# Kernel optimization log

Hardware: AMD Instinct MI355X
Metric: run time of the kernel (lower is better)

The kernel has to match this reference:

```python
import jax, jax.numpy as jnp
import numpy as np

B, T, D_OBS, D_ACT, H = 1024, 1024, 32, 4, 64


def setup_inputs() -> dict:
    key = jax.random.key(0)
    ks = jax.random.split(key, 8)
    s = 0.1
    obs = jax.random.normal(ks[0], (B, T, D_OBS), dtype=jnp.float32)
    action = jax.random.normal(ks[1], (B, T, D_ACT), dtype=jnp.float32)
    # GRUCell params (torch layout): weight_ih [3H, Din], weight_hh [3H, H]
    W_ih = jax.random.normal(ks[2], (3 * H, D_OBS + D_ACT), dtype=jnp.float32) * s
    W_hh = jax.random.normal(ks[3], (3 * H, H), dtype=jnp.float32) * s
    b_ih = jax.random.normal(ks[4], (3 * H,), dtype=jnp.float32) * s
    b_hh = jax.random.normal(ks[5], (3 * H,), dtype=jnp.float32) * s
    # reward head: Linear(H, 1)
    W_r = jax.random.normal(ks[6], (1, H), dtype=jnp.float32) * s
    b_r = jax.random.normal(ks[7], (1,), dtype=jnp.float32) * s
    return {"obs": obs, "action": action, "W_ih": W_ih, "b_ih": b_ih,
            "W_hh": W_hh, "b_hh": b_hh, "W_r": W_r, "b_r": b_r}


def reference(obs, action, W_ih, b_ih, W_hh, b_hh, W_r, b_r):
    # x_t = cat(obs_t, action_t); GRUCell recurrence; reward = Linear(h_t)
    x = jnp.concatenate([obs, action], axis=-1)              # [B, T, Din]
    # Precompute input-to-hidden gates for all timesteps (batched GEMM)
    gi = jnp.einsum('btd,gd->btg', x, W_ih) + b_ih           # [B, T, 3H]
    gi_t = jnp.swapaxes(gi, 0, 1)                            # [T, B, 3H]

    def step(h, gi_step):
        gh = h @ W_hh.T + b_hh                               # [B, 3H]
        ghr, ghz, ghn = jnp.split(gh, 3, axis=-1)
        gir, giz, gin = jnp.split(gi_step, 3, axis=-1)
        r = jax.nn.sigmoid(gir + ghr)
        z = jax.nn.sigmoid(giz + ghz)
        n = jnp.tanh(gin + r * ghn)
        h_new = (1.0 - z) * n + z * h
        reward = h_new @ W_r.T + b_r                         # [B, 1]
        return h_new, reward

    h0 = jnp.zeros((obs.shape[0], H), dtype=obs.dtype)
    h_final, rewards = jax.lax.scan(step, h0, gi_t)          # rewards: [T, B, 1]
    return h_final, jnp.swapaxes(rewards, 0, 1)              # h: [B, H], reward: [B, T, 1]
```

## Files before the change

kernel.cpp:

```cpp
#include <hip/hip_runtime.h>


#define BB 1024
#define TT 1024
#define DOBS 32
#define DACT 4
#define HH 64

typedef __attribute__((ext_vector_type(8))) short short8;
typedef __attribute__((ext_vector_type(4))) float f32x4;

#define MFMA(A, B, C) __builtin_amdgcn_mfma_f32_16x16x32_bf16((A), (B), (C), 0, 0, 0)

static __device__ __forceinline__ unsigned short f2bf(float f) {
    unsigned u = __float_as_uint(f);
    u += 0x7fffu + ((u >> 16) & 1u);
    return (unsigned short)(u >> 16);
}
static __device__ __forceinline__ float frcp(float x) { return __builtin_amdgcn_rcpf(x); }
static __device__ __forceinline__ unsigned cvt_pk(float lo, float hi) {
    unsigned r;
    asm("v_cvt_pk_bf16_f32 %0, %1, %2" : "=v"(r) : "v"(lo), "v"(hi));
    return r;
}

#define L2E 1.442695040888963f

__global__ __launch_bounds__(256)
void pack_x(const float* __restrict__ obs, const float* __restrict__ act,
            unsigned short* __restrict__ xext)
{
    const size_t r = (size_t)blockIdx.x * 256 + threadIdx.x;
    const float* o = obs + r * DOBS;
    unsigned short* d = xext + r * 40;
    short8 v[5];
#pragma unroll
    for (int j = 0; j < 4; ++j) {
        float4 a = ((const float4*)o)[2 * j];
        float4 b = ((const float4*)o)[2 * j + 1];
        short8 t;
        t[0]=f2bf(a.x); t[1]=f2bf(a.y); t[2]=f2bf(a.z); t[3]=f2bf(a.w);
        t[4]=f2bf(b.x); t[5]=f2bf(b.y); t[6]=f2bf(b.z); t[7]=f2bf(b.w);
        v[j] = t;
    }
    {
        float4 a = *(const float4*)(act + r * DACT);
        short8 t;
        t[0]=f2bf(a.x); t[1]=f2bf(a.y); t[2]=f2bf(a.z); t[3]=f2bf(a.w);
        t[4]=(short)0x3f80; t[5]=0; t[6]=0; t[7]=0;
        v[4] = t;
    }
#pragma unroll
    for (int j = 0; j < 5; ++j) ((short8*)d)[j] = v[j];
}

#define LOADX(XO, XA, T)                                                       \
  {                                                                            \
    if (PACKED) {                                                              \
      XO = *(const short8*)(px + (size_t)(T) * 40 + 8 * q);                    \
      XA = (q == 0) ? *(const short8*)(px + (size_t)(T) * 40 + 32) : zero8;    \
    } else {                                                                   \
      const int tc_ = (T) < TT ? (T) : TT - 1;                                 \
      const float* op_ = po + (size_t)tc_ * DOBS + 8 * q;                      \
      float4 a_ = *(const float4*)op_, b_ = *(const float4*)(op_ + 4);         \
      short8 f_;                                                               \
      f_[0]=f2bf(a_.x); f_[1]=f2bf(a_.y); f_[2]=f2bf(a_.z); f_[3]=f2bf(a_.w);  \
      f_[4]=f2bf(b_.x); f_[5]=f2bf(b_.y); f_[6]=f2bf(b_.z); f_[7]=f2bf(b_.w);  \
      XO = f_;                                                                 \
      if (q == 0) {                                                            \
        float4 av_ = *(const float4*)(pa + (size_t)tc_ * DACT);                \
        short8 g_;                                                             \
        g_[0]=f2bf(av_.x); g_[1]=f2bf(av_.y); g_[2]=f2bf(av_.z);               \
        g_[3]=f2bf(av_.w); g_[4]=(short)0x3f80; g_[5]=0; g_[6]=0; g_[7]=0;     \
        XA = g_;                                                               \
      } else XA = zero8;                                                       \
    }                                                                          \
  }

#define STEP(XO, XA, CR_, CZ_, CN_, PH, T)                                     \
  {                                                                            \
    short8 Ah0 = *(const short8*)((const char*)hbuf[PH] + rdaddr0);            \
    short8 Ah1 = *(const short8*)((const char*)hbuf[PH] + rdaddr1);            \
    f32x4 cr_ = CR_, cz_ = CZ_, cni_ = CN_;        \
    CR_ = MFMA(AX[0][1], XA, MFMA(AX[0][0], XO, zf));    \
    CZ_ = MFMA(AX[1][1], XA, MFMA(AX[1][0], XO, zf));                          \
    CN_ = MFMA(AX[2][1], XA, MFMA(AX[2][0], XO, zf));                          \
    LOADX(XO, XA, (T) + 4)                            \
    f32x4 Cr  = MFMA(AH[0][1], Ah1, MFMA(AH[0][0], Ah0, cr_));                 \
    f32x4 Cz  = MFMA(AH[1][1], Ah1, MFMA(AH[1][0], Ah0, cz_));                 \
    f32x4 Cnh = MFMA(AH[2][1], Ah1, MFMA(AH[2][0], Ah0, bhn4));                \
    f32x4 Crw = zf;                                                            \
    if (w == 3) Crw = MFMA(AR[1], Ah1, MFMA(AR[0], Ah0, zf));                  \
    _Pragma("unroll")                                                          \
    for (int reg = 0; reg < 4; ++reg) {                                        \
      float rr   = frcp(1.0f + __builtin_amdgcn_exp2f(Cr[reg]));               \
      float zz   = frcp(1.0f + __builtin_amdgcn_exp2f(Cz[reg]));               \
      float E    = __builtin_amdgcn_exp2f(__builtin_fmaf(rr, Cnh[reg], cni_[reg])); \
      float nn   = __builtin_fmaf(-2.0f, frcp(E + 1.0f), 1.0f);                \
      hold[reg]  = __builtin_fmaf(zz, hold[reg] - nn, nn);                     \
    }                                                                          \
    unsigned pk0 = cvt_pk(hold[0], hold[1]);                                   \
    unsigned pk1 = cvt_pk(hold[2], hold[3]);                                   \
    *(uint2*)((char*)hbuf[PH ^ 1] + wraddr) = make_uint2(pk0, pk1);            \
    if (w == 3 && q == 0 && (T) > 0)                                           \
      rew[(size_t)(bid * 16 + c) * TT + (T) - 1] = Crw[0] + brr;               \
    asm volatile("s_waitcnt lgkmcnt(0)" ::: "memory");                         \
    __builtin_amdgcn_s_barrier();                                              \
    asm volatile("" ::: "memory");                                             \
  }

template<bool PACKED>
__global__ __launch_bounds__(256, 1)
void gru_fused(const unsigned short* __restrict__ xext,
               const float* __restrict__ obs, const float* __restrict__ act,
               const float* __restrict__ W_ih, const float* __restrict__ b_ih,
               const float* __restrict__ W_hh, const float* __restrict__ b_hh,
               const float* __restrict__ W_r, const float* __restrict__ b_r,
               float* __restrict__ out)
{
    const int tid = threadIdx.x;
    const int w = tid >> 6, l = tid & 63, c = l & 15, q = l >> 4;
    const int bid = blockIdx.x;
    const int u0 = 16 * w + 4 * q;

    __shared__ __align__(16) unsigned short hbuf[2][16 * 64];

    short8 AX[3][2], AH[3][2];
#pragma unroll
    for (int m = 0; m < 3; ++m) {
        const float sc = (m == 2) ? (2.0f * L2E) : (-L2E);
        const int j = w + 4 * m;
        const int g = 16 * j + c;
        {
            const float* wp = W_ih + (size_t)g * 36 + 8 * q;
            float4 a = *(const float4*)wp, b = *(const float4*)(wp + 4);
            short8 f;
            f[0]=f2bf(a.x*sc); f[1]=f2bf(a.y*sc); f[2]=f2bf(a.z*sc); f[3]=f2bf(a.w*sc);
            f[4]=f2bf(b.x*sc); f[5]=f2bf(b.y*sc); f[6]=f2bf(b.z*sc); f[7]=f2bf(b.w*sc);
            AX[m][0] = f;
        }
        {
            short8 f;
#pragma unroll
            for (int i = 0; i < 8; ++i) {
                int k = 32 + 8 * q + i;
                float v = 0.f;
                if (k < 36)       v = W_ih[(size_t)g * 36 + k];
                else if (k == 36) v = b_ih[g] + (g < 128 ? b_hh[g] : 0.f);
                f[i] = f2bf(v * sc);
            }
            AX[m][1] = f;
        }
#pragma unroll
        for (int kk = 0; kk < 2; ++kk) {
            const float* wp = W_hh + (size_t)g * HH + 32 * kk + 8 * q;
            float4 a = *(const float4*)wp, b = *(const float4*)(wp + 4);
            short8 f;
            f[0]=f2bf(a.x*sc); f[1]=f2bf(a.y*sc); f[2]=f2bf(a.z*sc); f[3]=f2bf(a.w*sc);
            f[4]=f2bf(b.x*sc); f[5]=f2bf(b.y*sc); f[6]=f2bf(b.z*sc); f[7]=f2bf(b.w*sc);
            AH[m][kk] = f;
        }
    }
    short8 AR[2];
#pragma unroll
    for (int kk = 0; kk < 2; ++kk) {
        short8 f;
#pragma unroll
        for (int i = 0; i < 8; ++i) {
            int k = 32 * kk + 8 * q + i;
            f[i] = (c == 0) ? (short)f2bf(W_r[k]) : (short)0;
        }
        AR[kk] = f;
    }

    f32x4 bhn4;
#pragma unroll
    for (int reg = 0; reg < 4; ++reg) bhn4[reg] = b_hh[128 + u0 + reg] * (2.0f * L2E);
    const float brr = b_r[0];

    const int swz = c & 7;
    const int wraddr  = c * 128 + ((((u0 >> 3)) ^ swz) << 4) + (u0 & 7) * 2;
    const int rdaddr0 = c * 128 + ((q ^ swz) << 4);
    const int rdaddr1 = c * 128 + (((4 + q) ^ swz) << 4);

    const size_t row = (size_t)(bid * 16 + c) * TT;
    const unsigned short* px = xext + row * 40;
    const float* po = obs + row * DOBS;
    const float* pa = act + row * DACT;

    const short8 zero8 = {0, 0, 0, 0, 0, 0, 0, 0};
    const f32x4 zf = {0.f, 0.f, 0.f, 0.f};

    ((uint2*)hbuf[0])[tid] = make_uint2(0u, 0u);
    short8 xoA, xaA, xoB, xaB;
    LOADX(xoA, xaA, 0)
    LOADX(xoB, xaB, 1)
    f32x4 cgrA = MFMA(AX[0][1], xaA, MFMA(AX[0][0], xoA, zf));
    f32x4 cgzA = MFMA(AX[1][1], xaA, MFMA(AX[1][0], xoA, zf));
    f32x4 cgnA = MFMA(AX[2][1], xaA, MFMA(AX[2][0], xoA, zf));
    f32x4 cgrB = MFMA(AX[0][1], xaB, MFMA(AX[0][0], xoB, zf));
    f32x4 cgzB = MFMA(AX[1][1], xaB, MFMA(AX[1][0], xoB, zf));
    f32x4 cgnB = MFMA(AX[2][1], xaB, MFMA(AX[2][0], xoB, zf));
    LOADX(xoA, xaA, 2)
    LOADX(xoB, xaB, 3)
    float hold[4] = {0.f, 0.f, 0.f, 0.f};
    asm volatile("s_waitcnt lgkmcnt(0)" ::: "memory");
    __builtin_amdgcn_s_barrier();
    asm volatile("" ::: "memory");

    float* rew = out + (size_t)BB * HH;

#pragma unroll 1
    for (int t = 0; t < TT; t += 4) {
        STEP(xoA, xaA, cgrA, cgzA, cgnA, 0, t)
        STEP(xoB, xaB, cgrB, cgzB, cgnB, 1, t + 1)
        STEP(xoA, xaA, cgrA, cgzA, cgnA, 0, t + 2)
        STEP(xoB, xaB, cgrB, cgzB, cgnB, 1, t + 3)
    }

    if (w == 3) {
        short8 Ah0 = *(const short8*)((const char*)hbuf[0] + rdaddr0);
        short8 Ah1 = *(const short8*)((const char*)hbuf[0] + rdaddr1);
        f32x4 Crw = MFMA(AR[0], Ah0, zf);
        Crw = MFMA(AR[1], Ah1, Crw);
        if (q == 0)
            rew[(size_t)(bid * 16 + c) * TT + TT - 1] = Crw[0] + brr;
    }
    *(float4*)(out + (size_t)(bid * 16 + c) * HH + u0) =
        make_float4(hold[0], hold[1], hold[2], hold[3]);
}

extern "C" void kernel_launch(void* const* d_in, const int* in_sizes, int n_in,
                              void* d_out, int out_size, void* d_ws, size_t ws_size,
                              hipStream_t stream)
{
    const float* obs    = (const float*)d_in[0];
    const float* action = (const float*)d_in[1];
    const float* W_ih   = (const float*)d_in[2];
    const float* b_ih   = (const float*)d_in[3];
    const float* W_hh   = (const float*)d_in[4];
    const float* b_hh   = (const float*)d_in[5];
    const float* W_r    = (const float*)d_in[6];
    const float* b_r    = (const float*)d_in[7];
    float* out          = (float*)d_out;

    const size_t xext_bytes = ((size_t)BB * TT + 8) * 40 * sizeof(unsigned short);
    if (ws_size >= xext_bytes) {
        unsigned short* xext = (unsigned short*)d_ws;
        pack_x<<<dim3((BB * TT) / 256), dim3(256), 0, stream>>>(obs, action, xext);
        gru_fused<true><<<dim3(BB / 16), dim3(256), 0, stream>>>(
            xext, obs, action, W_ih, b_ih, W_hh, b_hh, W_r, b_r, out);
    } else {
        gru_fused<false><<<dim3(BB / 16), dim3(256), 0, stream>>>(
            nullptr, obs, action, W_ih, b_ih, W_hh, b_hh, W_r, b_r, out);
    }
}
```

Baseline: 415.3 us.

## Split GRU block into two alternating wave sets that ping-pong timesteps

Doubles the block to 512 threads, arranged as two 256-thread sets that take turns. One set runs the recurrent MFMA and gate step for one timestep while the other computes the input projection and loads x for its next step. The hidden state now moves between the sets through an extra fp32 shared buffer, because each set only holds every other step's state in registers. The reward-head work is also rotated across waves by iteration. The aim is to take input loads and projections off the serial critical path, at the cost of more LDS traffic and two barriers per timestep pair.

```diff
diff --git a/kernel.cpp b/kernel.cpp
--- a/kernel.cpp
+++ b/kernel.cpp
@@ -77,40 +77,44 @@
     }                                                                          \
   }
 
-#define STEP(XO, XA, CR_, CZ_, CN_, PH, T)                                     \
+#define HEAVY(PH, T, IT)                                                       \
   {                                                                            \
     short8 Ah0 = *(const short8*)((const char*)hbuf[PH] + rdaddr0);            \
     short8 Ah1 = *(const short8*)((const char*)hbuf[PH] + rdaddr1);            \
-    f32x4 cr_ = CR_, cz_ = CZ_, cni_ = CN_;        \
-    CR_ = MFMA(AX[0][1], XA, MFMA(AX[0][0], XO, zf));    \
-    CZ_ = MFMA(AX[1][1], XA, MFMA(AX[1][0], XO, zf));                          \
-    CN_ = MFMA(AX[2][1], XA, MFMA(AX[2][0], XO, zf));                          \
-    LOADX(XO, XA, (T) + 4)                            \
-    f32x4 Cr  = MFMA(AH[0][1], Ah1, MFMA(AH[0][0], Ah0, cr_));                 \
-    f32x4 Cz  = MFMA(AH[1][1], Ah1, MFMA(AH[1][0], Ah0, cz_));                 \
+    f32x4 hp = *(const f32x4*)((const char*)hf32[PH] + f32addr);               \
+    f32x4 Cr  = MFMA(AH[0][1], Ah1, MFMA(AH[0][0], Ah0, cgr));                 \
+    f32x4 Cz  = MFMA(AH[1][1], Ah1, MFMA(AH[1][0], Ah0, cgz));                 \
     f32x4 Cnh = MFMA(AH[2][1], Ah1, MFMA(AH[2][0], Ah0, bhn4));                \
     f32x4 Crw = zf;                                                            \
-    if (w == 3) Crw = MFMA(AR[1], Ah1, MFMA(AR[0], Ah0, zf));                  \
+    const bool dorw_ = (w == ((IT) & 3));                                      \
+    if (dorw_) Crw = MFMA(AR[1], Ah1, MFMA(AR[0], Ah0, zf));                   \
     _Pragma("unroll")                                                          \
     for (int reg = 0; reg < 4; ++reg) {                                        \
       float rr   = frcp(1.0f + __builtin_amdgcn_exp2f(Cr[reg]));               \
       float zz   = frcp(1.0f + __builtin_amdgcn_exp2f(Cz[reg]));               \
-      float E    = __builtin_amdgcn_exp2f(__builtin_fmaf(rr, Cnh[reg], cni_[reg])); \
+      float E    = __builtin_amdgcn_exp2f(__builtin_fmaf(rr, Cnh[reg], cgn[reg])); \
       float nn   = __builtin_fmaf(-2.0f, frcp(E + 1.0f), 1.0f);                \
-      hold[reg]  = __builtin_fmaf(zz, hold[reg] - nn, nn);                     \
+      hold[reg]  = __builtin_fmaf(zz, hp[reg] - nn, nn);                       \
     }                                                                          \
     unsigned pk0 = cvt_pk(hold[0], hold[1]);                                   \
     unsigned pk1 = cvt_pk(hold[2], hold[3]);                                   \
     *(uint2*)((char*)hbuf[PH ^ 1] + wraddr) = make_uint2(pk0, pk1);            \
-    if (w == 3 && q == 0 && (T) > 0)                                           \
+    *(f32x4*)((char*)hf32[PH ^ 1] + f32addr) = hold;                           \
+    if (dorw_ && q == 0 && (T) > 0)                                            \
       rew[(size_t)(bid * 16 + c) * TT + (T) - 1] = Crw[0] + brr;               \
     asm volatile("s_waitcnt lgkmcnt(0)" ::: "memory");                         \
-    __builtin_amdgcn_s_barrier();                                              \
-    asm volatile("" ::: "memory");                                             \
   }
 
+#define LIGHT(T2)                                                              \
+  {                                                                            \
+    cgr = MFMA(AX[0][1], xa, MFMA(AX[0][0], xo, zf));                          \
+    cgz = MFMA(AX[1][1], xa, MFMA(AX[1][0], xo, zf));                          \
+    cgn = MFMA(AX[2][1], xa, MFMA(AX[2][0], xo, zf));                          \
+    LOADX(xo, xa, (T2) + 2)                                                    \
+  }
+
 template<bool PACKED>
-__global__ __launch_bounds__(256, 1)
+__global__ __launch_bounds__(512, 1)
 void gru_fused(const unsigned short* __restrict__ xext,
                const float* __restrict__ obs, const float* __restrict__ act,
                const float* __restrict__ W_ih, const float* __restrict__ b_ih,
@@ -119,11 +123,14 @@
                float* __restrict__ out)
 {
     const int tid = threadIdx.x;
-    const int w = tid >> 6, l = tid & 63, c = l & 15, q = l >> 4;
+    const int set = tid >> 8;
+    const int w = (tid >> 6) & 3;
+    const int l = tid & 63, c = l & 15, q = l >> 4;
     const int bid = blockIdx.x;
     const int u0 = 16 * w + 4 * q;
 
     __shared__ __align__(16) unsigned short hbuf[2][16 * 64];
+    __shared__ __align__(16) float          hf32[2][16 * 64];
 
     short8 AX[3][2], AH[3][2];
 #pragma unroll
@@ -182,6 +189,7 @@
     const int wraddr  = c * 128 + ((((u0 >> 3)) ^ swz) << 4) + (u0 & 7) * 2;
     const int rdaddr0 = c * 128 + ((q ^ swz) << 4);
     const int rdaddr1 = c * 128 + (((4 + q) ^ swz) << 4);
+    const int f32addr = c * 256 + (((4 * w + q) ^ swz) << 4);
 
     const size_t row = (size_t)(bid * 16 + c) * TT;
     const unsigned short* px = xext + row * 40;
@@ -191,19 +199,20 @@
     const short8 zero8 = {0, 0, 0, 0, 0, 0, 0, 0};
     const f32x4 zf = {0.f, 0.f, 0.f, 0.f};
 
-    ((uint2*)hbuf[0])[tid] = make_uint2(0u, 0u);
-    short8 xoA, xaA, xoB, xaB;
-    LOADX(xoA, xaA, 0)
-    LOADX(xoB, xaB, 1)
-    f32x4 cgrA = MFMA(AX[0][1], xaA, MFMA(AX[0][0], xoA, zf));
-    f32x4 cgzA = MFMA(AX[1][1], xaA, MFMA(AX[1][0], xoA, zf));
-    f32x4 cgnA = MFMA(AX[2][1], xaA, MFMA(AX[2][0], xoA, zf));
-    f32x4 cgrB = MFMA(AX[0][1], xaB, MFMA(AX[0][0], xoB, zf));
-    f32x4 cgzB = MFMA(AX[1][1], xaB, MFMA(AX[1][0], xoB, zf));
-    f32x4 cgnB = MFMA(AX[2][1], xaB, MFMA(AX[2][0], xoB, zf));
-    LOADX(xoA, xaA, 2)
-    LOADX(xoB, xaB, 3)
-    float hold[4] = {0.f, 0.f, 0.f, 0.f};
+    ((uint2*)hbuf)[tid] = make_uint2(0u, 0u);
+    ((f32x4*)hf32)[tid] = zf;
+    short8 xo, xa;
+    f32x4 cgr = zf, cgz = zf, cgn = zf;
+    if (set == 0) {
+        LOADX(xo, xa, 0)
+        cgr = MFMA(AX[0][1], xa, MFMA(AX[0][0], xo, zf));
+        cgz = MFMA(AX[1][1], xa, MFMA(AX[1][0], xo, zf));
+        cgn = MFMA(AX[2][1], xa, MFMA(AX[2][0], xo, zf));
+        LOADX(xo, xa, 2)
+    } else {
+        LOADX(xo, xa, 1)
+    }
+    f32x4 hold = zf;
     asm volatile("s_waitcnt lgkmcnt(0)" ::: "memory");
     __builtin_amdgcn_s_barrier();
     asm volatile("" ::: "memory");
@@ -211,23 +220,28 @@
     float* rew = out + (size_t)BB * HH;
 
 #pragma unroll 1
-    for (int t = 0; t < TT; t += 4) {
-        STEP(xoA, xaA, cgrA, cgzA, cgnA, 0, t)
-        STEP(xoB, xaB, cgrB, cgzB, cgnB, 1, t + 1)
-        STEP(xoA, xaA, cgrA, cgzA, cgnA, 0, t + 2)
-        STEP(xoB, xaB, cgrB, cgzB, cgnB, 1, t + 3)
-    }
-
-    if (w == 3) {
-        short8 Ah0 = *(const short8*)((const char*)hbuf[0] + rdaddr0);
-        short8 Ah1 = *(const short8*)((const char*)hbuf[0] + rdaddr1);
-        f32x4 Crw = MFMA(AR[0], Ah0, zf);
-        Crw = MFMA(AR[1], Ah1, Crw);
-        if (q == 0)
-            rew[(size_t)(bid * 16 + c) * TT + TT - 1] = Crw[0] + brr;
-    }
-    *(float4*)(out + (size_t)(bid * 16 + c) * HH + u0) =
-        make_float4(hold[0], hold[1], hold[2], hold[3]);
+    for (int it = 0; it < TT / 2; ++it) {
+        const int Ta = 2 * it, Tb = 2 * it + 1;
+        if (set == 0) { HEAVY(0, Ta, it) } else { LIGHT(Tb) }
+        __builtin_amdgcn_s_barrier();
+        asm volatile("" ::: "memory");
+        if (set == 1) { HEAVY(1, Tb, it) } else { LIGHT(Ta + 2) }
+        __builtin_amdgcn_s_barrier();
+        asm volatile("" ::: "memory");
+    }
+
+    if (set == 1) {
+        if (w == 3) {
+            short8 Ah0 = *(const short8*)((const char*)hbuf[0] + rdaddr0);
+            short8 Ah1 = *(const short8*)((const char*)hbuf[0] + rdaddr1);
+            f32x4 Crw = MFMA(AR[0], Ah0, zf);
+            Crw = MFMA(AR[1], Ah1, Crw);
+            if (q == 0)
+                rew[(size_t)(bid * 16 + c) * TT + TT - 1] = Crw[0] + brr;
+        }
+        *(float4*)(out + (size_t)(bid * 16 + c) * HH + u0) =
+            make_float4(hold[0], hold[1], hold[2], hold[3]);
+    }
 }
 
 extern "C" void kernel_launch(void* const* d_in, const int* in_sizes, int n_in,
@@ -248,10 +262,10 @@
     if (ws_size >= xext_bytes) {
         unsigned short* xext = (unsigned short*)d_ws;
         pack_x<<<dim3((BB * TT) / 256), dim3(256), 0, stream>>>(obs, action, xext);
-        gru_fused<true><<<dim3(BB / 16), dim3(256), 0, stream>>>(
+        gru_fused<true><<<dim3(BB / 16), dim3(512), 0, stream>>>(
             xext, obs, action, W_ih, b_ih, W_hh, b_hh, W_r, b_r, out);
     } else {
-        gru_fused<false><<<dim3(BB / 16), dim3(256), 0, stream>>>(
+        gru_fused<false><<<dim3(BB / 16), dim3(512), 0, stream>>>(
             nullptr, obs, action, W_ih, b_ih, W_hh, b_hh, W_r, b_r, out);
     }
 }
```

New measurement: 399.8 us. 3.7% less time.
